# Kernel optimization log

Measured on AMD Instinct MI355X. Metric: run time of the kernel, lower is better.

Reference implementation:

```python
import jax, jax.numpy as jnp
import numpy as np

NUM_HEADS = 16
NUM_KV_HEADS = 4
HEAD_DIM = 128
HALF_DIM = HEAD_DIM // 2
LAMBDA_INIT = 0.8
LAMBDA_MIN = 0.0
LAMBDA_MAX = 1.0
CAUSAL = True
NORMALIZE_DIFF = True
NEG = -1.0e9


def setup_inputs() -> dict:
    key = jax.random.key(0)
    k1, k2, k3 = jax.random.split(key, 3)
    B, Sq, Sk = 1, 2048, 2048
    query = jax.random.normal(k1, (B, NUM_HEADS, Sq, HEAD_DIM), dtype=jnp.float32)
    key_t = jax.random.normal(k2, (B, NUM_KV_HEADS, Sk, HEAD_DIM), dtype=jnp.float32)
    value = jax.random.normal(k3, (B, NUM_KV_HEADS, Sk, HEAD_DIM), dtype=jnp.float32)
    return {"query": query, "key": key_t, "value": value}


def reference(query, key, value):
    scale = 1.0 / (HALF_DIM ** 0.5)
    lam = jnp.clip(jnp.float32(LAMBDA_INIT), LAMBDA_MIN, LAMBDA_MAX)
    # GQA: repeat KV heads to match query heads
    rep = NUM_HEADS // NUM_KV_HEADS
    k = jnp.repeat(key, rep, axis=1)    # [b,h,k,d]
    v = jnp.repeat(value, rep, axis=1)  # [b,h,k,d]
    q1, q2 = query[..., :HALF_DIM], query[..., HALF_DIM:]
    k1, k2 = k[..., :HALF_DIM], k[..., HALF_DIM:]
    scores1 = jnp.einsum('bhqd,bhkd->bhqk', q1, k1) * scale
    scores2 = jnp.einsum('bhqd,bhkd->bhqk', q2, k2) * scale
    if CAUSAL:
        Sq, Sk = query.shape[2], k.shape[2]
        mask = jnp.tril(jnp.ones((Sq, Sk), dtype=jnp.float32))  # lower-triangular causal
        scores1 = scores1 * mask + (1.0 - mask) * NEG
        scores2 = scores2 * mask + (1.0 - mask) * NEG
    attn1 = jax.nn.softmax(scores1, axis=-1)
    attn2 = jax.nn.softmax(scores2, axis=-1)
    diff_attn = attn1 - lam * attn2
    out = jnp.einsum('bhqk,bhkd->bhqd', diff_attn, v)
    if NORMALIZE_DIFF:
        out = out * (1.0 - LAMBDA_INIT)
    return out
```

## Files before the change

### kernel.cpp

```cpp
#include <hip/hip_runtime.h>

#define NUM_HEADS 16
#define HEAD_DIM  128
#define SEQ       2048

typedef __attribute__((ext_vector_type(8))) unsigned short us8;
typedef __attribute__((ext_vector_type(8))) __bf16 bf16x8;
typedef __attribute__((ext_vector_type(4))) float f32x4;
typedef __attribute__((ext_vector_type(4))) unsigned u32x4;
typedef __attribute__((ext_vector_type(2))) unsigned u32x2;

static __device__ inline unsigned short f2bf(float x) {
    union { float f; unsigned u; } v; v.f = x;
    unsigned r = v.u + 0x7FFFu + ((v.u >> 16) & 1u);
    return (unsigned short)(r >> 16);
}
static __device__ inline float bf2f(unsigned short h) {
    union { float f; unsigned u; } v; v.u = ((unsigned)h) << 16;
    return v.f;
}
static __device__ inline unsigned pk2bf(float a, float b) {
    return (unsigned)f2bf(a) | ((unsigned)f2bf(b) << 16);
}
static __device__ inline f32x4 mfma16(us8 a, us8 b, f32x4 c) {
    return __builtin_amdgcn_mfma_f32_16x16x32_bf16(
        __builtin_bit_cast(bf16x8, a), __builtin_bit_cast(bf16x8, b), c, 0, 0, 0);
}

__global__ __launch_bounds__(256)
void prep_kv(const float* __restrict__ K, const float* __restrict__ V,
             unsigned short* __restrict__ Kbf, unsigned short* __restrict__ Vtb)
{
    const int bx = (int)blockIdx.x, t = (int)threadIdx.x;
    __shared__ __align__(16) float Ls[64][130];
    if (bx < 512) {
        const size_t base = ((size_t)bx * 256 + t) * 8;
        float x[8];
        *(float4*)&x[0] = *(const float4*)(K + base);
        *(float4*)&x[4] = *(const float4*)(K + base + 4);
        u32x4 pk;
        #pragma unroll
        for (int j = 0; j < 4; ++j) pk[j] = pk2bf(x[2*j], x[2*j+1]);
        *(us8*)(Kbf + base) = __builtin_bit_cast(us8, pk);
    } else {
        const int b2 = bx - 512, kvh = b2 >> 5, tile = b2 & 31;
        const float* vb = V + ((size_t)kvh * SEQ + tile * 64) * HEAD_DIM;
        #pragma unroll
        for (int i = 0; i < 8; ++i) {
            const int idx = t + i * 256;
            const int r = idx >> 5, c4 = idx & 31;
            *(float4*)&Ls[r][c4 * 4] = *(const float4*)(vb + (size_t)r * HEAD_DIM + c4 * 4);
        }
        __syncthreads();
        const int d = t & 127, kh = t >> 7;
        unsigned pk[16];
        #pragma unroll
        for (int j = 0; j < 16; ++j)
            pk[j] = pk2bf(Ls[kh * 32 + 2*j][d], Ls[kh * 32 + 2*j + 1][d]);
        unsigned short* dst = Vtb + ((size_t)(kvh * 32 + tile) * 128 + d) * 64 + kh * 32;
        #pragma unroll
        for (int blk = 0; blk < 4; ++blk)
            *(us8*)(dst + blk * 8) = *(us8*)&pk[blk * 4];
    }
}

#define KS_OFF 0
#define VT_OFF 16384
#define P_OFF  32768

__global__ __launch_bounds__(256, 3)
void diff_attn_mfma4(const float* __restrict__ Q,
                     const unsigned short* __restrict__ Kbf,
                     const unsigned short* __restrict__ Vtb,
                     float* __restrict__ Out)
{
    __shared__ __align__(16) unsigned char smem[41984];

    const int t    = (int)threadIdx.x;
    const int wv   = t >> 6;
    const int ln   = t & 63;
    const int l15  = ln & 15;
    const int quad = ln >> 4;
    const int mat  = wv >> 1;
    const int rfh  = wv & 1;

    const int bx  = (int)blockIdx.x;
    const int h   = bx & 15;
    const int idx = bx >> 4;
    const int qt  = (idx < 32) ? idx : 95 - idx;
    const int kvh = h >> 2;
    const int q0  = qt * 32;
    const int nkt = (qt >> 1) + 1;

    us8 qhi[2], qlo[2];
    {
        const float* qr = Q + ((size_t)h * SEQ + q0 + rfh * 16 + l15) * HEAD_DIM + mat * 64;
        #pragma unroll
        for (int kc = 0; kc < 2; ++kc) {
            const int d0 = kc * 32 + quad * 8;
            float x[8];
            *(float4*)&x[0] = *(const float4*)(qr + d0);
            *(float4*)&x[4] = *(const float4*)(qr + d0 + 4);
            us8 hi8, lo8;
            #pragma unroll
            for (int j = 0; j < 8; ++j) {
                float xs = x[j] * 0.125f;
                unsigned short hb = f2bf(xs);
                hi8[j] = hb;
                lo8[j] = f2bf(xs - bf2f(hb));
            }
            qhi[kc] = hi8; qlo[kc] = lo8;
        }
    }

    f32x4 o[8];
    #pragma unroll
    for (int i = 0; i < 8; ++i) o[i] = (f32x4)0.f;
    float rs = 0.f;

    const unsigned short* Kt0 = Kbf + (size_t)kvh * SEQ * HEAD_DIM;
    const unsigned short* Vt0 = Vtb + (size_t)kvh * 32 * 128 * 64;
    unsigned char* Pp = smem + P_OFF + wv * 2304;

    for (int kt = 0; kt < nkt; ++kt) {
        __syncthreads();

        #pragma unroll
        for (int i = 0; i < 4; ++i) {
            const int L  = i * 256 + wv * 64 + ln;
            const int r  = L >> 4;
            const int ch = (L & 15) ^ (r & 15);
            const unsigned short* g = Kt0 + (size_t)(kt * 64 + r) * 128 + ch * 8;
            __builtin_amdgcn_global_load_lds(
                (const __attribute__((address_space(1))) unsigned*)g,
                (__attribute__((address_space(3))) unsigned*)(smem + KS_OFF + (i * 256 + wv * 64) * 16),
                16, 0, 0);
        }
        #pragma unroll
        for (int i = 0; i < 4; ++i) {
            const int L  = i * 256 + wv * 64 + ln;
            const int r  = L >> 3;
            const int ch = (L & 7) ^ (r & 7);
            const unsigned short* g = Vt0 + (size_t)(kt * 128 + r) * 64 + ch * 8;
            __builtin_amdgcn_global_load_lds(
                (const __attribute__((address_space(1))) unsigned*)g,
                (__attribute__((address_space(3))) unsigned*)(smem + VT_OFF + (i * 256 + wv * 64) * 16),
                16, 0, 0);
        }
        __syncthreads();

        #pragma unroll
        for (int c4 = 0; c4 < 4; ++c4) {
            f32x4 s = (f32x4)0.f;
            #pragma unroll
            for (int kc = 0; kc < 2; ++kc) {
                const int r  = c4 * 16 + l15;
                const int ch = (mat * 8 + kc * 4 + quad) ^ l15;
                us8 ak = *(const us8*)(smem + KS_OFF + r * 256 + ch * 16);
                s = mfma16(ak, qhi[kc], s);
                s = mfma16(ak, qlo[kc], s);
            }
            const int kg0 = kt * 64 + c4 * 16 + quad * 4;
            const int qg  = q0 + rfh * 16 + l15;
            unsigned tr[4];
            #pragma unroll
            for (int rg = 0; rg < 4; ++rg) {
                const bool ok = (kg0 + rg) <= qg;
                float ev = ok ? __expf(s[rg]) : 0.f;
                tr[rg] = __builtin_bit_cast(unsigned, ev) & 0xffff0000u;
                rs += __builtin_bit_cast(float, tr[rg]);
            }
            u32x2 pw;
            pw[0] = (tr[0] >> 16) | tr[1];
            pw[1] = (tr[2] >> 16) | tr[3];
            *(u32x2*)(Pp + l15 * 144 + c4 * 32 + quad * 8) = pw;
        }

        asm volatile("s_waitcnt lgkmcnt(0)" ::: "memory");

        #pragma unroll
        for (int c2 = 0; c2 < 2; ++c2) {
            us8 bp = *(const us8*)(Pp + l15 * 144 + c2 * 64 + quad * 16);
            #pragma unroll
            for (int dt = 0; dt < 8; ++dt) {
                const int r  = dt * 16 + l15;
                const int ch = (c2 * 4 + quad) ^ (r & 7);
                us8 av = *(const us8*)(smem + VT_OFF + r * 128 + ch * 16);
                o[dt] = mfma16(av, bp, o[dt]);
            }
        }
    }

    __syncthreads();

    rs += __shfl_xor(rs, 16, 64);
    rs += __shfl_xor(rs, 32, 64);
    const float inv = 1.0f / rs;

    float* Cb = (float*)smem;
    if (mat == 1) {
        #pragma unroll
        for (int dt = 0; dt < 8; ++dt) {
            f32x4 v;
            #pragma unroll
            for (int rg = 0; rg < 4; ++rg) v[rg] = o[dt][rg] * inv;
            *(f32x4*)(Cb + (rfh * 16 + l15) * 132 + dt * 16 + quad * 4) = v;
        }
    }
    __syncthreads();
    if (mat == 0) {
        float* ob = Out + ((size_t)h * SEQ + q0 + rfh * 16 + l15) * HEAD_DIM;
        #pragma unroll
        for (int dt = 0; dt < 8; ++dt) {
            const float* cb = Cb + (rfh * 16 + l15) * 132 + dt * 16 + quad * 4;
            float4 r;
            r.x = 0.2f * (o[dt][0] * inv) - 0.16f * cb[0];
            r.y = 0.2f * (o[dt][1] * inv) - 0.16f * cb[1];
            r.z = 0.2f * (o[dt][2] * inv) - 0.16f * cb[2];
            r.w = 0.2f * (o[dt][3] * inv) - 0.16f * cb[3];
            *(float4*)(ob + dt * 16 + quad * 4) = r;
        }
    }
}

extern "C" void kernel_launch(void* const* d_in, const int* in_sizes, int n_in,
                              void* d_out, int out_size, void* d_ws, size_t ws_size,
                              hipStream_t stream) {
    const float* Q = (const float*)d_in[0];
    const float* K = (const float*)d_in[1];
    const float* V = (const float*)d_in[2];
    float* Out = (float*)d_out;

    unsigned short* Kbf = (unsigned short*)d_ws;
    unsigned short* Vtb = Kbf + (size_t)4 * SEQ * HEAD_DIM;

    prep_kv<<<640, 256, 0, stream>>>(K, V, Kbf, Vtb);
    diff_attn_mfma4<<<1024, 256, 0, stream>>>(Q, Kbf, Vtb, Out);
}
```

Baseline: 126.9 us.

## Double-buffer K/V tiles in LDS and use exp2 with last-tile-only masking

New measurement: 124.8 us. No clear change (-1.7%).

```diff
diff --git a/kernel.cpp b/kernel.cpp
--- a/kernel.cpp
+++ b/kernel.cpp
@@ -21,6 +21,13 @@
 }
 static __device__ inline unsigned pk2bf(float a, float b) {
     return (unsigned)f2bf(a) | ((unsigned)f2bf(b) << 16);
+}
+static __device__ inline float fast_exp2(float x) {
+#if __has_builtin(__builtin_amdgcn_exp2f)
+    return __builtin_amdgcn_exp2f(x);
+#else
+    return exp2f(x);
+#endif
 }
 static __device__ inline f32x4 mfma16(us8 a, us8 b, f32x4 c) {
     return __builtin_amdgcn_mfma_f32_16x16x32_bf16(
@@ -64,17 +71,19 @@
     }
 }
 
-#define KS_OFF 0
-#define VT_OFF 16384
-#define P_OFF  32768
-
-__global__ __launch_bounds__(256, 3)
-void diff_attn_mfma4(const float* __restrict__ Q,
+#define KB0 0
+#define KB1 16384
+#define VB0 32768
+#define VB1 49152
+#define P_OFF 65536
+
+__global__ __launch_bounds__(256, 2)
+void diff_attn_mfma5(const float* __restrict__ Q,
                      const unsigned short* __restrict__ Kbf,
                      const unsigned short* __restrict__ Vtb,
                      float* __restrict__ Out)
 {
-    __shared__ __align__(16) unsigned char smem[41984];
+    __shared__ __align__(16) unsigned char smem[74752];
 
     const int t    = (int)threadIdx.x;
     const int wv   = t >> 6;
@@ -95,6 +104,7 @@
     us8 qhi[2], qlo[2];
     {
         const float* qr = Q + ((size_t)h * SEQ + q0 + rfh * 16 + l15) * HEAD_DIM + mat * 64;
+        const float qscale = 0.125f * 1.44269504088896340736f;
         #pragma unroll
         for (int kc = 0; kc < 2; ++kc) {
             const int d0 = kc * 32 + quad * 8;
@@ -104,7 +114,7 @@
             us8 hi8, lo8;
             #pragma unroll
             for (int j = 0; j < 8; ++j) {
-                float xs = x[j] * 0.125f;
+                float xs = x[j] * qscale;
                 unsigned short hb = f2bf(xs);
                 hi8[j] = hb;
                 lo8[j] = f2bf(xs - bf2f(hb));
@@ -116,15 +126,13 @@
     f32x4 o[8];
     #pragma unroll
     for (int i = 0; i < 8; ++i) o[i] = (f32x4)0.f;
-    float rs = 0.f;
+    f32x4 rsv = (f32x4)0.f;
 
     const unsigned short* Kt0 = Kbf + (size_t)kvh * SEQ * HEAD_DIM;
     const unsigned short* Vt0 = Vtb + (size_t)kvh * 32 * 128 * 64;
     unsigned char* Pp = smem + P_OFF + wv * 2304;
 
-    for (int kt = 0; kt < nkt; ++kt) {
-        __syncthreads();
-
+    auto issue = [&](int kt, int koff, int voff) {
         #pragma unroll
         for (int i = 0; i < 4; ++i) {
             const int L  = i * 256 + wv * 64 + ln;
@@ -133,7 +141,7 @@
             const unsigned short* g = Kt0 + (size_t)(kt * 64 + r) * 128 + ch * 8;
             __builtin_amdgcn_global_load_lds(
                 (const __attribute__((address_space(1))) unsigned*)g,
-                (__attribute__((address_space(3))) unsigned*)(smem + KS_OFF + (i * 256 + wv * 64) * 16),
+                (__attribute__((address_space(3))) unsigned*)(smem + koff + (i * 256 + wv * 64) * 16),
                 16, 0, 0);
         }
         #pragma unroll
@@ -144,10 +152,22 @@
             const unsigned short* g = Vt0 + (size_t)(kt * 128 + r) * 64 + ch * 8;
             __builtin_amdgcn_global_load_lds(
                 (const __attribute__((address_space(1))) unsigned*)g,
-                (__attribute__((address_space(3))) unsigned*)(smem + VT_OFF + (i * 256 + wv * 64) * 16),
+                (__attribute__((address_space(3))) unsigned*)(smem + voff + (i * 256 + wv * 64) * 16),
                 16, 0, 0);
         }
+    };
+
+    issue(0, KB0, VB0);
+
+    for (int kt = 0; kt < nkt; ++kt) {
+        const int cur = kt & 1;
         __syncthreads();
+
+        if (kt + 1 < nkt) issue(kt + 1, cur ? KB0 : KB1, cur ? VB0 : VB1);
+
+        const unsigned char* kbase = smem + (cur ? KB1 : KB0);
+        const unsigned char* vbase = smem + (cur ? VB1 : VB0);
+        const bool lastkt = (kt == nkt - 1);
 
         #pragma unroll
         for (int c4 = 0; c4 < 4; ++c4) {
@@ -156,19 +176,27 @@
             for (int kc = 0; kc < 2; ++kc) {
                 const int r  = c4 * 16 + l15;
                 const int ch = (mat * 8 + kc * 4 + quad) ^ l15;
-                us8 ak = *(const us8*)(smem + KS_OFF + r * 256 + ch * 16);
+                us8 ak = *(const us8*)(kbase + r * 256 + ch * 16);
                 s = mfma16(ak, qhi[kc], s);
                 s = mfma16(ak, qlo[kc], s);
             }
-            const int kg0 = kt * 64 + c4 * 16 + quad * 4;
-            const int qg  = q0 + rfh * 16 + l15;
+            float ev[4];
+            if (lastkt) {
+                const int kg0 = kt * 64 + c4 * 16 + quad * 4;
+                const int qg  = q0 + rfh * 16 + l15;
+                #pragma unroll
+                for (int rg = 0; rg < 4; ++rg)
+                    ev[rg] = ((kg0 + rg) <= qg) ? fast_exp2(s[rg]) : 0.f;
+            } else {
+                #pragma unroll
+                for (int rg = 0; rg < 4; ++rg)
+                    ev[rg] = fast_exp2(s[rg]);
+            }
             unsigned tr[4];
             #pragma unroll
             for (int rg = 0; rg < 4; ++rg) {
-                const bool ok = (kg0 + rg) <= qg;
-                float ev = ok ? __expf(s[rg]) : 0.f;
-                tr[rg] = __builtin_bit_cast(unsigned, ev) & 0xffff0000u;
-                rs += __builtin_bit_cast(float, tr[rg]);
+                tr[rg] = __builtin_bit_cast(unsigned, ev[rg]) & 0xffff0000u;
+                rsv[rg] += __builtin_bit_cast(float, tr[rg]);
             }
             u32x2 pw;
             pw[0] = (tr[0] >> 16) | tr[1];
@@ -185,7 +213,7 @@
             for (int dt = 0; dt < 8; ++dt) {
                 const int r  = dt * 16 + l15;
                 const int ch = (c2 * 4 + quad) ^ (r & 7);
-                us8 av = *(const us8*)(smem + VT_OFF + r * 128 + ch * 16);
+                us8 av = *(const us8*)(vbase + r * 128 + ch * 16);
                 o[dt] = mfma16(av, bp, o[dt]);
             }
         }
@@ -193,6 +221,7 @@
 
     __syncthreads();
 
+    float rs = (rsv[0] + rsv[1]) + (rsv[2] + rsv[3]);
     rs += __shfl_xor(rs, 16, 64);
     rs += __shfl_xor(rs, 32, 64);
     const float inv = 1.0f / rs;
@@ -235,5 +264,5 @@
     unsigned short* Vtb = Kbf + (size_t)4 * SEQ * HEAD_DIM;
 
     prep_kv<<<640, 256, 0, stream>>>(K, V, Kbf, Vtb);
-    diff_attn_mfma4<<<1024, 256, 0, stream>>>(Q, Kbf, Vtb, Out);
-}
+    diff_attn_mfma5<<<1024, 256, 0, stream>>>(Q, Kbf, Vtb, Out);
+}
```
